# Optimization experiments

Measured on AMD Instinct MI355X. Metric: run time of the kernel, lower is better.

## Reference

```python
import jax, jax.numpy as jnp
import numpy as np

B, N, DIM = 4, 2048, 1024
HEADS, DIM_HEAD = 16, 64
INNER = HEADS * DIM_HEAD


def setup_inputs() -> dict:
    key = jax.random.key(0)
    kx, kw = jax.random.split(key)
    x = jax.random.normal(kx, (B, N, DIM), dtype=jnp.float32)
    # Dense kernel [in_features, out_features], no bias
    w_qkv = jax.random.normal(kw, (DIM, 3 * INNER), dtype=jnp.float32) * (DIM ** -0.5)
    return {"x": x, "w_qkv": w_qkv}


def reference(x, w_qkv):
    scale = DIM_HEAD ** (-0.5)
    qkv = jnp.einsum('bnc,cf->bnf', x, w_qkv)  # [B, N, 3*INNER]
    q, k, v = jnp.split(qkv, 3, axis=-1)
    # 'b n (h d) -> b h n d'
    def to_heads(t):
        return t.reshape(B, N, HEADS, DIM_HEAD).transpose(0, 2, 1, 3)
    q, k, v = map(to_heads, (q, k, v))
    dots = jnp.einsum('bhid,bhjd->bhij', q, k) * scale  # [B, H, N, N]
    attn = jax.nn.softmax(dots, axis=-1)
    out = jnp.einsum('bhij,bhjd->bhid', attn, v)  # [B, H, N, D]
    # 'b h n d -> b n (h d)'
    return out.transpose(0, 2, 1, 3).reshape(B, N, INNER)
```

## Files before the change

kernel.cpp:

```cpp
#include <hip/hip_runtime.h>
#include <hip/hip_bf16.h>
#include <math.h>

typedef __bf16 bf16x4 __attribute__((ext_vector_type(4)));
typedef __bf16 bf16x8 __attribute__((ext_vector_type(8)));
typedef float f32x4 __attribute__((ext_vector_type(4)));

#define MFMA16(a, b, c) __builtin_amdgcn_mfma_f32_16x16x32_bf16(a, b, c, 0, 0, 0)
#define QSCALE 0.1803368801111204f

__device__ __forceinline__ void gload_lds16(const __bf16* g, __bf16* l) {
  __builtin_amdgcn_global_load_lds((const __attribute__((address_space(1))) void*)g,
                                   (__attribute__((address_space(3))) void*)l,
                                   16, 0, 0);
}

__global__ __launch_bounds__(256) void convert_x(const float* __restrict__ in,
                                                 __bf16* __restrict__ out) {
  int i = blockIdx.x * 256 + threadIdx.x;
  float4 v = ((const float4*)in)[i];
  bf16x4 o = {(__bf16)v.x, (__bf16)v.y, (__bf16)v.z, (__bf16)v.w};
  *(bf16x4*)&out[i * 4] = o;
}

__global__ __launch_bounds__(256) void transpose_w(const float* __restrict__ W,
                                                   __bf16* __restrict__ Wt) {
  __shared__ __bf16 tile[64][65];
  const int bx = blockIdx.x;
  const int by = blockIdx.y;
  const int t = threadIdx.x;
  const int lr = t >> 6;
  const int lc = t & 63;
  const float sc = (bx < 16) ? QSCALE : 1.0f;
#pragma unroll
  for (int i = 0; i < 16; ++i) {
    int r = lr + i * 4;
    tile[r][lc] = (__bf16)(W[(size_t)(by * 64 + r) * 3072 + bx * 64 + lc] * sc);
  }
  __syncthreads();
#pragma unroll
  for (int i = 0; i < 16; ++i) {
    int r = lr + i * 4;
    Wt[(size_t)(bx * 64 + r) * 1024 + by * 64 + lc] = tile[lc][r];
  }
}

__global__ __launch_bounds__(256) void gemm_qkv(const __bf16* __restrict__ X,
                                                const __bf16* __restrict__ Wt,
                                                __bf16* __restrict__ QKV) {
  __shared__ __bf16 As[128 * 32];
  __shared__ __bf16 Bs[128 * 32];
  const int t = threadIdx.x;
  const int lane = t & 63;
  const int wave = t >> 6;
  const int quad = lane >> 4;
  const int l16 = lane & 15;
  const int n0 = blockIdx.x * 128;
  const int m0 = blockIdx.y * 128;
  const int wm = (wave & 1) * 64;
  const int wn = (wave >> 1) * 64;

  const __bf16* Ag = &X[(size_t)(m0 + wave * 16 + (lane >> 2)) * 1024 + (lane & 3) * 8];
  const __bf16* Bg = &Wt[(size_t)(n0 + wave * 16 + (lane >> 2)) * 1024 + (lane & 3) * 8];
  __bf16* As0 = &As[wave * 512];
  __bf16* As1 = &As[2048 + wave * 512];
  __bf16* Bs0 = &Bs[wave * 512];
  __bf16* Bs1 = &Bs[2048 + wave * 512];

  f32x4 acc[4][4] = {};

  for (int k0 = 0; k0 < 1024; k0 += 32) {
    gload_lds16(Ag + k0, As0);
    gload_lds16(Ag + (size_t)64 * 1024 + k0, As1);
    gload_lds16(Bg + k0, Bs0);
    gload_lds16(Bg + (size_t)64 * 1024 + k0, Bs1);
    __syncthreads();

    bf16x8 af[4], bf[4];
#pragma unroll
    for (int mi = 0; mi < 4; ++mi)
      af[mi] = *(const bf16x8*)&As[(wm + mi * 16 + l16) * 32 + quad * 8];
#pragma unroll
    for (int ni = 0; ni < 4; ++ni)
      bf[ni] = *(const bf16x8*)&Bs[(wn + ni * 16 + l16) * 32 + quad * 8];
#pragma unroll
    for (int mi = 0; mi < 4; ++mi)
#pragma unroll
      for (int ni = 0; ni < 4; ++ni)
        acc[mi][ni] = MFMA16(af[mi], bf[ni], acc[mi][ni]);
    __syncthreads();
  }

#pragma unroll
  for (int mi = 0; mi < 4; ++mi)
#pragma unroll
    for (int ni = 0; ni < 4; ++ni)
#pragma unroll
      for (int r = 0; r < 4; ++r) {
        int row = m0 + wm + mi * 16 + quad * 4 + r;
        int col = n0 + wn + ni * 16 + l16;
        QKV[(size_t)row * 3072 + col] = (__bf16)acc[mi][ni][r];
      }
}

__global__ __launch_bounds__(256) void transpose_v(const __bf16* __restrict__ QKV,
                                                   __bf16* __restrict__ Vt) {
  __shared__ __bf16 tile[64][65];
  const int k0 = blockIdx.x * 64;
  const int h = blockIdx.y;
  const int b = blockIdx.z;
  const int t = threadIdx.x;
  const int lr = t >> 6;
  const int lc = t & 63;
  const __bf16* src = QKV + (size_t)b * 2048 * 3072 + 2048 + h * 64;
  __bf16* dst = Vt + (size_t)(b * 16 + h) * 64 * 2048;
#pragma unroll
  for (int i = 0; i < 16; ++i) {
    int r = lr + i * 4;
    tile[r][lc] = src[(size_t)(k0 + r) * 3072 + lc];
  }
  __syncthreads();
#pragma unroll
  for (int i = 0; i < 16; ++i) {
    int d = lr + i * 4;
    dst[(size_t)d * 2048 + k0 + lc] = tile[lc][d];
  }
}

#define AT_LD 72

__global__ __launch_bounds__(256) void attn(const __bf16* __restrict__ QKV,
                                            const __bf16* __restrict__ Vt,
                                            float* __restrict__ Out) {
  const int h = blockIdx.y;
  const int b = blockIdx.z;
  const int t = threadIdx.x;
  const int lane = t & 63;
  const int wave = t >> 6;
  const int quad = lane >> 4;
  const int l16 = lane & 15;
  const int q0w = blockIdx.x * 128 + wave * 32;

  const size_t base = (size_t)b * 2048 * 3072;
  const __bf16* Qb = QKV + base + h * 64;
  const __bf16* Kb = QKV + base + 1024 + h * 64;
  const __bf16* Vtb = Vt + (size_t)(b * 16 + h) * 64 * 2048;

  __shared__ __bf16 Ks[64 * AT_LD];
  __shared__ __bf16 Vs[64 * AT_LD];
  __shared__ __bf16 Ps[4][32 * AT_LD];
  __bf16* Psw = Ps[wave];

  bf16x8 qf[2][2];
#pragma unroll
  for (int mi = 0; mi < 2; ++mi)
#pragma unroll
    for (int kc = 0; kc < 2; ++kc)
      qf[mi][kc] = *(const bf16x8*)&Qb[(size_t)(q0w + mi * 16 + l16) * 3072 + kc * 32 + quad * 8];

  f32x4 o[2][4] = {};
  float lsum[2] = {0.0f, 0.0f};

  const int srow = t >> 2;
  const int sc = (t & 3) * 16;

  for (int kv0 = 0; kv0 < 2048; kv0 += 64) {
    bf16x8 k0v = *(const bf16x8*)&Kb[(size_t)(kv0 + srow) * 3072 + sc];
    bf16x8 k1v = *(const bf16x8*)&Kb[(size_t)(kv0 + srow) * 3072 + sc + 8];
    bf16x8 v0v = *(const bf16x8*)&Vtb[(size_t)srow * 2048 + kv0 + sc];
    bf16x8 v1v = *(const bf16x8*)&Vtb[(size_t)srow * 2048 + kv0 + sc + 8];
    __syncthreads();
    *(bf16x8*)&Ks[srow * AT_LD + sc] = k0v;
    *(bf16x8*)&Ks[srow * AT_LD + sc + 8] = k1v;
    *(bf16x8*)&Vs[srow * AT_LD + sc] = v0v;
    *(bf16x8*)&Vs[srow * AT_LD + sc + 8] = v1v;
    __syncthreads();

#pragma unroll
    for (int mt = 0; mt < 4; ++mt) {
      bf16x8 kf0 = *(const bf16x8*)&Ks[(mt * 16 + l16) * AT_LD + quad * 8];
      bf16x8 kf1 = *(const bf16x8*)&Ks[(mt * 16 + l16) * AT_LD + 32 + quad * 8];
#pragma unroll
      for (int mi = 0; mi < 2; ++mi) {
        f32x4 z = {};
        z = MFMA16(kf0, qf[mi][0], z);
        z = MFMA16(kf1, qf[mi][1], z);
        bf16x4 pk;
#pragma unroll
        for (int r = 0; r < 4; ++r) {
          float p = __builtin_amdgcn_exp2f(z[r]);
          lsum[mi] += p;
          pk[r] = (__bf16)p;
        }
        *(bf16x4*)&Psw[(mi * 16 + l16) * AT_LD + mt * 16 + quad * 4] = pk;
      }
    }

    bf16x8 pf[2][2];
#pragma unroll
    for (int mi = 0; mi < 2; ++mi)
#pragma unroll
      for (int kc = 0; kc < 2; ++kc)
        pf[mi][kc] = *(const bf16x8*)&Psw[(mi * 16 + l16) * AT_LD + kc * 32 + quad * 8];

#pragma unroll
    for (int dt = 0; dt < 4; ++dt) {
      bf16x8 vf0 = *(const bf16x8*)&Vs[(dt * 16 + l16) * AT_LD + quad * 8];
      bf16x8 vf1 = *(const bf16x8*)&Vs[(dt * 16 + l16) * AT_LD + 32 + quad * 8];
#pragma unroll
      for (int mi = 0; mi < 2; ++mi) {
        o[mi][dt] = MFMA16(pf[mi][0], vf0, o[mi][dt]);
        o[mi][dt] = MFMA16(pf[mi][1], vf1, o[mi][dt]);
      }
    }
  }

#pragma unroll
  for (int mi = 0; mi < 2; ++mi) {
    lsum[mi] += __shfl_xor(lsum[mi], 16);
    lsum[mi] += __shfl_xor(lsum[mi], 32);
  }

#pragma unroll
  for (int mi = 0; mi < 2; ++mi)
#pragma unroll
    for (int r = 0; r < 4; ++r) {
      float inv = 1.0f / __shfl(lsum[mi], quad * 4 + r);
      int orow = b * 2048 + q0w + mi * 16 + quad * 4 + r;
#pragma unroll
      for (int dt = 0; dt < 4; ++dt)
        Out[(size_t)orow * 1024 + h * 64 + dt * 16 + l16] = o[mi][dt][r] * inv;
    }
}

extern "C" void kernel_launch(void* const* d_in, const int* in_sizes, int n_in,
                              void* d_out, int out_size, void* d_ws, size_t ws_size,
                              hipStream_t stream) {
  const float* x = (const float*)d_in[0];
  const float* w = (const float*)d_in[1];
  float* out = (float*)d_out;

  __bf16* Wt = (__bf16*)d_ws;
  __bf16* QKV = Wt + (size_t)3072 * 1024;
  __bf16* Xb = QKV + (size_t)8192 * 3072;
  __bf16* Vtr = Xb;

  convert_x<<<8192, 256, 0, stream>>>(x, Xb);
  transpose_w<<<dim3(48, 16), 256, 0, stream>>>(w, Wt);
  gemm_qkv<<<dim3(24, 64), 256, 0, stream>>>(Xb, Wt, QKV);
  transpose_v<<<dim3(32, 16, 4), 256, 0, stream>>>(QKV, Vtr);
  attn<<<dim3(16, 16, 4), 256, 0, stream>>>(QKV, Vtr, out);
}
```

Before: 253.9 us.

## Switch attention to 32x32 MFMA and keep P in registers via lane shuffles

Rewrites the attention inner loop to use 32x32x16 bf16 MFMA tiles instead of 16x16x32, with each wave handling 32 queries as a single tile. The exponentiated scores are repacked into the A-operand layout for the PV product using cross-half lane shuffles, so the per-wave shared-memory staging of P is no longer needed. This is meant to cut LDS traffic and per-MFMA operand loads, but it adds shuffle and select work and raises register pressure from the 16-wide accumulators.

```diff
diff --git a/kernel.cpp b/kernel.cpp
--- a/kernel.cpp
+++ b/kernel.cpp
@@ -2,17 +2,29 @@
 #include <hip/hip_bf16.h>
 #include <math.h>
 
+typedef __bf16 bf16x2 __attribute__((ext_vector_type(2)));
 typedef __bf16 bf16x4 __attribute__((ext_vector_type(4)));
 typedef __bf16 bf16x8 __attribute__((ext_vector_type(8)));
 typedef float f32x4 __attribute__((ext_vector_type(4)));
+typedef float f32x16 __attribute__((ext_vector_type(16)));
 
 #define MFMA16(a, b, c) __builtin_amdgcn_mfma_f32_16x16x32_bf16(a, b, c, 0, 0, 0)
+#define MFMA32(a, b, c) __builtin_amdgcn_mfma_f32_32x32x16_bf16(a, b, c, 0, 0, 0)
 #define QSCALE 0.1803368801111204f
 
 __device__ __forceinline__ void gload_lds16(const __bf16* g, __bf16* l) {
   __builtin_amdgcn_global_load_lds((const __attribute__((address_space(1))) void*)g,
                                    (__attribute__((address_space(3))) void*)l,
                                    16, 0, 0);
+}
+
+__device__ __forceinline__ bf16x2 shflx32(bf16x2 x) {
+  int i;
+  __builtin_memcpy(&i, &x, 4);
+  i = __shfl_xor(i, 32);
+  bf16x2 r;
+  __builtin_memcpy(&r, &i, 4);
+  return r;
 }
 
 __global__ __launch_bounds__(256) void convert_x(const float* __restrict__ in,
@@ -137,8 +149,8 @@
   const int t = threadIdx.x;
   const int lane = t & 63;
   const int wave = t >> 6;
-  const int quad = lane >> 4;
-  const int l16 = lane & 15;
+  const int l31 = lane & 31;
+  const int half = lane >> 5;
   const int q0w = blockIdx.x * 128 + wave * 32;
 
   const size_t base = (size_t)b * 2048 * 3072;
@@ -148,18 +160,14 @@
 
   __shared__ __bf16 Ks[64 * AT_LD];
   __shared__ __bf16 Vs[64 * AT_LD];
-  __shared__ __bf16 Ps[4][32 * AT_LD];
-  __bf16* Psw = Ps[wave];
-
-  bf16x8 qf[2][2];
-#pragma unroll
-  for (int mi = 0; mi < 2; ++mi)
-#pragma unroll
-    for (int kc = 0; kc < 2; ++kc)
-      qf[mi][kc] = *(const bf16x8*)&Qb[(size_t)(q0w + mi * 16 + l16) * 3072 + kc * 32 + quad * 8];
-
-  f32x4 o[2][4] = {};
-  float lsum[2] = {0.0f, 0.0f};
+
+  bf16x8 qf[4];
+#pragma unroll
+  for (int dc = 0; dc < 4; ++dc)
+    qf[dc] = *(const bf16x8*)&Qb[(size_t)(q0w + l31) * 3072 + dc * 16 + half * 8];
+
+  f32x16 o[2] = {};
+  float lsum = 0.0f;
 
   const int srow = t >> 2;
   const int sc = (t & 3) * 16;
@@ -176,60 +184,70 @@
     *(bf16x8*)&Vs[srow * AT_LD + sc + 8] = v1v;
     __syncthreads();
 
-#pragma unroll
-    for (int mt = 0; mt < 4; ++mt) {
-      bf16x8 kf0 = *(const bf16x8*)&Ks[(mt * 16 + l16) * AT_LD + quad * 8];
-      bf16x8 kf1 = *(const bf16x8*)&Ks[(mt * 16 + l16) * AT_LD + 32 + quad * 8];
-#pragma unroll
-      for (int mi = 0; mi < 2; ++mi) {
-        f32x4 z = {};
-        z = MFMA16(kf0, qf[mi][0], z);
-        z = MFMA16(kf1, qf[mi][1], z);
-        bf16x4 pk;
-#pragma unroll
-        for (int r = 0; r < 4; ++r) {
-          float p = __builtin_amdgcn_exp2f(z[r]);
-          lsum[mi] += p;
-          pk[r] = (__bf16)p;
+    bf16x2 pp[2][4][2];
+#pragma unroll
+    for (int kt = 0; kt < 2; ++kt) {
+      f32x16 c = {};
+#pragma unroll
+      for (int dc = 0; dc < 4; ++dc) {
+        bf16x8 kf = *(const bf16x8*)&Ks[(kt * 32 + l31) * AT_LD + dc * 16 + half * 8];
+        c = MFMA32(kf, qf[dc], c);
+      }
+#pragma unroll
+      for (int g = 0; g < 4; ++g)
+#pragma unroll
+        for (int p = 0; p < 2; ++p) {
+          float e0 = __builtin_amdgcn_exp2f(c[g * 4 + p * 2]);
+          float e1 = __builtin_amdgcn_exp2f(c[g * 4 + p * 2 + 1]);
+          lsum += e0 + e1;
+          pp[kt][g][p] = bf16x2{(__bf16)e0, (__bf16)e1};
         }
-        *(bf16x4*)&Psw[(mi * 16 + l16) * AT_LD + mt * 16 + quad * 4] = pk;
+    }
+
+    bf16x8 pf[4];
+#pragma unroll
+    for (int kk = 0; kk < 4; ++kk) {
+      const int kt = kk >> 1;
+      const int g0 = (2 * kk) & 3;
+      const int g1 = (2 * kk + 1) & 3;
+      bf16x2 x0 = pp[kt][g0][0], x1 = pp[kt][g0][1];
+      bf16x2 y0 = pp[kt][g1][0], y1 = pp[kt][g1][1];
+      bf16x2 a0 = half ? y0 : x0;
+      bf16x2 a1 = half ? y1 : x1;
+      bf16x2 r0 = shflx32(half ? x0 : y0);
+      bf16x2 r1 = shflx32(half ? x1 : y1);
+      union { bf16x8 v; bf16x2 hh[4]; } f;
+      f.hh[0] = half ? r0 : a0;
+      f.hh[1] = half ? r1 : a1;
+      f.hh[2] = half ? a0 : r0;
+      f.hh[3] = half ? a1 : r1;
+      pf[kk] = f.v;
+    }
+
+#pragma unroll
+    for (int dt = 0; dt < 2; ++dt)
+#pragma unroll
+      for (int kk = 0; kk < 4; ++kk) {
+        bf16x8 vf = *(const bf16x8*)&Vs[(dt * 32 + l31) * AT_LD + kk * 16 + half * 8];
+        o[dt] = MFMA32(pf[kk], vf, o[dt]);
       }
-    }
-
-    bf16x8 pf[2][2];
-#pragma unroll
-    for (int mi = 0; mi < 2; ++mi)
-#pragma unroll
-      for (int kc = 0; kc < 2; ++kc)
-        pf[mi][kc] = *(const bf16x8*)&Psw[(mi * 16 + l16) * AT_LD + kc * 32 + quad * 8];
-
-#pragma unroll
-    for (int dt = 0; dt < 4; ++dt) {
-      bf16x8 vf0 = *(const bf16x8*)&Vs[(dt * 16 + l16) * AT_LD + quad * 8];
-      bf16x8 vf1 = *(const bf16x8*)&Vs[(dt * 16 + l16) * AT_LD + 32 + quad * 8];
-#pragma unroll
-      for (int mi = 0; mi < 2; ++mi) {
-        o[mi][dt] = MFMA16(pf[mi][0], vf0, o[mi][dt]);
-        o[mi][dt] = MFMA16(pf[mi][1], vf1, o[mi][dt]);
-      }
-    }
-  }
-
-#pragma unroll
-  for (int mi = 0; mi < 2; ++mi) {
-    lsum[mi] += __shfl_xor(lsum[mi], 16);
-    lsum[mi] += __shfl_xor(lsum[mi], 32);
-  }
-
-#pragma unroll
-  for (int mi = 0; mi < 2; ++mi)
-#pragma unroll
-    for (int r = 0; r < 4; ++r) {
-      float inv = 1.0f / __shfl(lsum[mi], quad * 4 + r);
-      int orow = b * 2048 + q0w + mi * 16 + quad * 4 + r;
-#pragma unroll
-      for (int dt = 0; dt < 4; ++dt)
-        Out[(size_t)orow * 1024 + h * 64 + dt * 16 + l16] = o[mi][dt][r] * inv;
+  }
+
+  lsum += __shfl_xor(lsum, 32);
+  float inv = 1.0f / lsum;
+
+  float iv[16];
+#pragma unroll
+  for (int r = 0; r < 16; ++r)
+    iv[r] = __shfl(inv, (r & 3) + 8 * (r >> 2) + 4 * half);
+
+#pragma unroll
+  for (int dt = 0; dt < 2; ++dt)
+#pragma unroll
+    for (int r = 0; r < 16; ++r) {
+      int qr = (r & 3) + 8 * (r >> 2) + 4 * half;
+      Out[(size_t)(b * 2048 + q0w + qr) * 1024 + h * 64 + dt * 32 + l31] =
+          o[dt][r] * iv[r];
     }
 }
 
```

Result: slower. 263.5 us (+3.8%).
